# Kernel optimization log

Hardware: AMD Instinct MI355X
Metric: run time of the kernel (lower is better)

Reference implementation:

```python
import jax, jax.numpy as jnp
import numpy as np

M_PLUS, M_MINUS, LAMBDA = 0.9, 0.1, 0.5
NUM_CLASSES = 21
IGNORE = 255


def setup_inputs() -> dict:
    key = jax.random.key(0)
    k1, k2 = jax.random.split(key)
    class_caps = jax.random.normal(k1, (8, NUM_CLASSES, 16), dtype=jnp.float32)
    raw = jax.random.randint(k2, (8, 512, 512), 0, NUM_CLASSES + 1).astype(jnp.int32)
    # value NUM_CLASSES acts as the ignore label (255), exercising the ignore path
    labels = jnp.where(raw == NUM_CLASSES, IGNORE, raw).astype(jnp.int32)
    return {"class_caps": class_caps, "labels": labels}


def reference(class_caps, labels):
    B = class_caps.shape[0]
    C = NUM_CLASSES
    # capsule lengths: [B, C]
    caps_lengths = jnp.sqrt(jnp.sum(class_caps ** 2, axis=2))

    lbl = labels.reshape(B, -1)                       # [B, P]
    ignore = lbl == IGNORE
    lbl_clean = jnp.where(ignore, 0, lbl)
    valid = (~ignore).astype(jnp.float32)

    # image-level multi-label presence: max over valid pixels of one-hot labels,
    # done as a scatter-max instead of materializing a [B, P, C] one-hot tensor.
    bidx = jnp.broadcast_to(jnp.arange(B)[:, None], lbl.shape)
    image_labels = jnp.zeros((B, C), jnp.float32).at[bidx, lbl_clean].max(valid)

    left = jax.nn.relu(M_PLUS - caps_lengths) ** 2
    right = jax.nn.relu(caps_lengths - M_MINUS) ** 2
    margin = image_labels * left + LAMBDA * (1.0 - image_labels) * right
    margin_loss = jnp.mean(jnp.sum(margin, axis=1))

    margin_loss_weight = 1.0
    total_loss = margin_loss_weight * margin_loss
    return total_loss
```

## Files before the change

kernel.cpp:

```cpp
#include <hip/hip_runtime.h>
#include <hip/hip_bf16.h>

#define NUM_CLASSES 21
#define LAMBDA 0.5f

__global__ __launch_bounds__(256) void caps_fused1(
        const int* __restrict__ labels, const float* __restrict__ caps,
        unsigned* __restrict__ bm, float* __restrict__ lr) {
    int t = threadIdx.x;
    if (blockIdx.x < 256) {
        const int4* L = reinterpret_cast<const int4*>(labels)
                        + (size_t)blockIdx.x * 2048;
        unsigned m = 0;
        #pragma unroll
        for (int k = 0; k < 8; ++k) {
            int4 v = L[t + k * 256];
            if ((unsigned)v.x < (unsigned)NUM_CLASSES) m |= 1u << v.x;
            if ((unsigned)v.y < (unsigned)NUM_CLASSES) m |= 1u << v.y;
            if ((unsigned)v.z < (unsigned)NUM_CLASSES) m |= 1u << v.z;
            if ((unsigned)v.w < (unsigned)NUM_CLASSES) m |= 1u << v.w;
        }
        #pragma unroll
        for (int s = 1; s < 64; s <<= 1) m |= __shfl_xor(m, s, 64);
        if ((t & 63) == 0) bm[blockIdx.x * 4 + (t >> 6)] = m;
    } else {
        if (t < 8 * NUM_CLASSES) {
            const float* p = caps + t * 16;
            float s2 = 0.0f;
            #pragma unroll
            for (int d = 0; d < 16; ++d) { float x = p[d]; s2 += x * x; }
            float len = sqrtf(s2);
            float l = fmaxf(0.9f - len, 0.0f);  l *= l;
            float r = fmaxf(len - 0.1f, 0.0f);  r *= r;
            lr[t] = l;
            lr[168 + t] = r;
        }
    }
}

__global__ __launch_bounds__(256) void caps_finalize(
        const unsigned* __restrict__ bm, const float* __restrict__ lr,
        float* __restrict__ out) {
    __shared__ unsigned pres[8];
    __shared__ float psum[4];
    int t = threadIdx.x;
    int b = t >> 5, j = t & 31;
    unsigned m = 0;
    const unsigned* p = bm + b * 128 + j * 4;
    #pragma unroll
    for (int k = 0; k < 4; ++k) m |= p[k];
    #pragma unroll
    for (int s = 16; s; s >>= 1) m |= __shfl_xor(m, s, 64);
    if (j == 0) pres[b] = m;
    __syncthreads();

    float v = 0.0f;
    if (t < 8 * NUM_CLASSES) {
        int bb = t / NUM_CLASSES, c = t % NUM_CLASSES;
        v = ((pres[bb] >> c) & 1u) ? lr[t] : LAMBDA * lr[168 + t];
    }
    #pragma unroll
    for (int s = 32; s; s >>= 1) v += __shfl_xor(v, s, 64);
    if ((t & 63) == 0) psum[t >> 6] = v;
    __syncthreads();
    if (t == 0) out[0] = (psum[0] + psum[1] + psum[2] + psum[3]) * 0.125f;
}

extern "C" void kernel_launch(void* const* d_in, const int* in_sizes, int n_in,
                              void* d_out, int out_size, void* d_ws, size_t ws_size,
                              hipStream_t stream) {
    const float* caps   = (const float*)d_in[0];
    const int*   labels = (const int*)d_in[1];
    float* out = (float*)d_out;
    unsigned* bm = (unsigned*)d_ws;
    float* lr = (float*)((char*)d_ws + 4096);

    caps_fused1<<<257, 256, 0, stream>>>(labels, caps, bm, lr);
    caps_finalize<<<1, 256, 0, stream>>>(bm, lr, out);
}
```

Before: 11.23 us.

## Fuse finalize into single kernel using atomic signature handshake between blocks

Merges the two kernels into one launch. The last block computes the capsule margins itself, then spins with atomicExch on each workspace word until it sees the signature tag written by the label-scanning blocks. It resets each word to a sentinel so the next call starts clean. This removes the second kernel launch and the workspace round trip for the margin terms, but it depends on the spinning block never starving the producer blocks and adds polling and atomic traffic.

Result: slower. 11.65 us (+3.8%).

```diff
diff --git a/kernel.cpp b/kernel.cpp
--- a/kernel.cpp
+++ b/kernel.cpp
@@ -1,12 +1,16 @@
 #include <hip/hip_runtime.h>
 #include <hip/hip_bf16.h>
 
-#define NUM_CLASSES 21
+#define NC 21
 #define LAMBDA 0.5f
 
-__global__ __launch_bounds__(256) void caps_fused1(
+#define SIG  0x2B3u
+#define SIGW (SIG << 21)
+#define SENT 0x80000000u
+
+__global__ __launch_bounds__(256) void caps_fused(
         const int* __restrict__ labels, const float* __restrict__ caps,
-        unsigned* __restrict__ bm, float* __restrict__ lr) {
+        unsigned* bm, float* __restrict__ out) {
     int t = threadIdx.x;
     if (blockIdx.x < 256) {
         const int4* L = reinterpret_cast<const int4*>(labels)
@@ -15,49 +19,53 @@
         #pragma unroll
         for (int k = 0; k < 8; ++k) {
             int4 v = L[t + k * 256];
-            if ((unsigned)v.x < (unsigned)NUM_CLASSES) m |= 1u << v.x;
-            if ((unsigned)v.y < (unsigned)NUM_CLASSES) m |= 1u << v.y;
-            if ((unsigned)v.z < (unsigned)NUM_CLASSES) m |= 1u << v.z;
-            if ((unsigned)v.w < (unsigned)NUM_CLASSES) m |= 1u << v.w;
+            if ((unsigned)v.x < (unsigned)NC) m |= 1u << v.x;
+            if ((unsigned)v.y < (unsigned)NC) m |= 1u << v.y;
+            if ((unsigned)v.z < (unsigned)NC) m |= 1u << v.z;
+            if ((unsigned)v.w < (unsigned)NC) m |= 1u << v.w;
         }
         #pragma unroll
         for (int s = 1; s < 64; s <<= 1) m |= __shfl_xor(m, s, 64);
-        if ((t & 63) == 0) bm[blockIdx.x * 4 + (t >> 6)] = m;
-    } else {
-        if (t < 8 * NUM_CLASSES) {
-            const float* p = caps + t * 16;
-            float s2 = 0.0f;
-            #pragma unroll
-            for (int d = 0; d < 16; ++d) { float x = p[d]; s2 += x * x; }
-            float len = sqrtf(s2);
-            float l = fmaxf(0.9f - len, 0.0f);  l *= l;
-            float r = fmaxf(len - 0.1f, 0.0f);  r *= r;
-            lr[t] = l;
-            lr[168 + t] = r;
+        if ((t & 63) == 0)
+            atomicExch(bm + blockIdx.x * 4 + (t >> 6), m | SIGW);
+        return;
+    }
+
+    float l = 0.0f, r = 0.0f;
+    if (t < 8 * NC) {
+        const float* p = caps + t * 16;
+        float s2 = 0.0f;
+        #pragma unroll
+        for (int d = 0; d < 16; ++d) { float x = p[d]; s2 += x * x; }
+        float len = sqrtf(s2);
+        l = fmaxf(0.9f - len, 0.0f);  l *= l;
+        r = fmaxf(len - 0.1f, 0.0f);  r *= r;
+    }
+
+    unsigned acc = 0, got = 0;
+    unsigned* base = bm + t * 4;
+    while (got != 0xFu) {
+        #pragma unroll
+        for (int k = 0; k < 4; ++k) {
+            if (!(got & (1u << k))) {
+                unsigned v = atomicExch(base + k, SENT);
+                if ((v >> 21) == SIG) { acc |= v & 0x1FFFFFu; got |= 1u << k; }
+            }
         }
+        if (got != 0xFu) __builtin_amdgcn_s_sleep(1);
     }
-}
 
-__global__ __launch_bounds__(256) void caps_finalize(
-        const unsigned* __restrict__ bm, const float* __restrict__ lr,
-        float* __restrict__ out) {
+    #pragma unroll
+    for (int s = 16; s; s >>= 1) acc |= __shfl_xor(acc, s, 64);
     __shared__ unsigned pres[8];
     __shared__ float psum[4];
-    int t = threadIdx.x;
-    int b = t >> 5, j = t & 31;
-    unsigned m = 0;
-    const unsigned* p = bm + b * 128 + j * 4;
-    #pragma unroll
-    for (int k = 0; k < 4; ++k) m |= p[k];
-    #pragma unroll
-    for (int s = 16; s; s >>= 1) m |= __shfl_xor(m, s, 64);
-    if (j == 0) pres[b] = m;
+    if ((t & 31) == 0) pres[t >> 5] = acc;
     __syncthreads();
 
     float v = 0.0f;
-    if (t < 8 * NUM_CLASSES) {
-        int bb = t / NUM_CLASSES, c = t % NUM_CLASSES;
-        v = ((pres[bb] >> c) & 1u) ? lr[t] : LAMBDA * lr[168 + t];
+    if (t < 8 * NC) {
+        int bb = t / NC, c = t % NC;
+        v = ((pres[bb] >> c) & 1u) ? l : LAMBDA * r;
     }
     #pragma unroll
     for (int s = 32; s; s >>= 1) v += __shfl_xor(v, s, 64);
@@ -73,8 +81,6 @@
     const int*   labels = (const int*)d_in[1];
     float* out = (float*)d_out;
     unsigned* bm = (unsigned*)d_ws;
-    float* lr = (float*)((char*)d_ws + 4096);
 
-    caps_fused1<<<257, 256, 0, stream>>>(labels, caps, bm, lr);
-    caps_finalize<<<1, 256, 0, stream>>>(bm, lr, out);
+    caps_fused<<<257, 256, 0, stream>>>(labels, caps, bm, out);
 }
```
